# Kernel tuning notes

Hardware: AMD Instinct MI355X
Metric: run time of the kernel (lower is better)

The kernel has to match this reference:

```python
import jax, jax.numpy as jnp
import numpy as np

SHARPNESS = 1000.0   # sigmoid temperature from source: *1000.0
BIAS = 0.008         # shadow acne bias from source: -0.008
FILTER_SIZE = 1      # 3x3 PCF
SHADOW_STEP = 1


def setup_inputs() -> dict:
    key = jax.random.key(0)
    k1, k2, k3 = jax.random.split(key, 3)
    N, H, W, K, S = 8, 1024, 1024, 1, 2048
    # light-view depth buffer (fragments_from_light.zbuf), K=1 squeezed
    light_zbuf = jax.random.uniform(k1, (N, S, S), dtype=jnp.float32)
    depth_z = jax.random.uniform(k2, (N, H, W, K), dtype=jnp.float32)
    # rounded integer light-screen coords per camera pixel: [..., 0]=x, [..., 1]=y
    xy = jax.random.randint(k3, (N, H, W, K, 2), 0, S, dtype=jnp.int32)
    return {"light_zbuf": light_zbuf, "depth_z": depth_z, "xy": xy, "image_size": S}


def reference(light_zbuf, depth_z, xy, image_size):
    N, H, W, K = depth_z.shape
    b = jnp.arange(N, dtype=jnp.int32)[:, None, None, None]  # broadcast batch index
    x = xy[..., 0]  # [N,H,W,K]
    y = xy[..., 1]
    aa = depth_z - BIAS
    vis = jnp.zeros_like(depth_z)
    # 3x3 PCF: gather clamped neighbors in the light zbuf, soft depth test, accumulate
    for ii in range(-FILTER_SIZE, FILTER_SIZE + 1):
        for jj in range(-FILTER_SIZE, FILTER_SIZE + 1):
            yi = jnp.clip(y + ii * SHADOW_STEP, 0, image_size - 1)
            xi = jnp.clip(x + jj * SHADOW_STEP, 0, image_size - 1)
            bb = light_zbuf[b, yi, xi]  # [N,H,W,K] gather
            vis = vis + jax.nn.sigmoid((bb - aa) * SHARPNESS)
    return vis / float((1 + 2 * FILTER_SIZE) ** 2)
```

## Files before the change

### kernel.cpp

```cpp
#include <hip/hip_runtime.h>


#define SHARPNESS 1000.0f
#define BIAS 0.008f
#define S2LOG2E 1442.6950408889634f

#define S_IMG   2048
#define NBATCH  8
#define HWK     (1 << 20)
#define TSH     6
#define TPS     32
#define BPB     (TPS * TPS)
#define CAP     1408
#define RPT     6
#define STW     66
#define PXB     16384
#define P1T     1024
#define PPT     (PXB / P1T)
#define BLKB    (HWK / PXB)
#define SENT    0xFFFFFFFFu

typedef int      i4v __attribute__((ext_vector_type(4)));
typedef float    f2v __attribute__((ext_vector_type(2)));
typedef float    f4v __attribute__((ext_vector_type(4)));
typedef unsigned u2v __attribute__((ext_vector_type(2)));
typedef unsigned u4v __attribute__((ext_vector_type(4)));

__device__ __forceinline__ float sigf(float bb, float a) {
    const float t = (a - bb) * S2LOG2E;
    return __builtin_amdgcn_rcpf(1.0f + exp2f(t));
}

__global__ __launch_bounds__(P1T, 1) void p1_bin(
    const int* __restrict__ xy_raw, const float* __restrict__ depth,
    u2v* __restrict__ slab, float* __restrict__ out ,
    unsigned* __restrict__ gcur, int b0)
{
    __shared__ u2v      srec[PXB];
    __shared__ unsigned scn[BPB];
    __shared__ unsigned lbase[BPB];
    __shared__ unsigned gbse[BPB];

    const int blk = blockIdx.x;
    const int bl  = blk >> 6;
    const int sub = blk & (BLKB - 1);
    const int tid = threadIdx.x;
    scn[tid] = 0;
    __syncthreads();

    const size_t pb_g = (size_t)(b0 + bl) * HWK + (size_t)sub * PXB;
    const i4v* xq = (const i4v*)xy_raw + pb_g / 2;
    const f2v* dq = (const f2v*)depth  + pb_g / 2;

    unsigned pk[PPT]; float dd[PPT];
#pragma unroll
    for (int j = 0; j < PPT / 2; ++j) {
        const i4v q = __builtin_nontemporal_load(&xq[j * P1T + tid]);
        const f2v d = __builtin_nontemporal_load(&dq[j * P1T + tid]);
        pk[2 * j]     = (unsigned)q.x | ((unsigned)q.y << 11);
        pk[2 * j + 1] = (unsigned)q.z | ((unsigned)q.w << 11);
        dd[2 * j] = d.x; dd[2 * j + 1] = d.y;
        atomicAdd(&scn[((q.y >> TSH) << 5) | (q.x >> TSH)], 1u);
        atomicAdd(&scn[((q.w >> TSH) << 5) | (q.z >> TSH)], 1u);
    }
    __syncthreads();

    const unsigned creg = scn[tid];
    for (int ofs = 1; ofs < BPB; ofs <<= 1) {
        const unsigned u = (tid >= ofs) ? scn[tid - ofs] : 0u;
        __syncthreads();
        scn[tid] += u;
        __syncthreads();
    }
    const unsigned lb = scn[tid] - creg;
    lbase[tid] = lb;
    gbse[tid]  = atomicAdd(&gcur[(b0 + bl) * BPB + tid], (creg + 7u) & ~7u);
    scn[tid]   = lb;
    __syncthreads();

    u2v* px2 = (u2v*)(out + pb_g);
#pragma unroll
    for (int j = 0; j < PPT / 2; ++j) {
        u2v pi;
#pragma unroll
        for (int e = 0; e < 2; ++e) {
            const unsigned w = pk[2 * j + e];
            const int x = (int)(w & 0x7FFu), y = (int)(w >> 11);
            const int bn = ((y >> TSH) << 5) | (x >> TSH);
            const unsigned r = atomicAdd(&scn[bn], 1u);
            u2v rec;
            rec.x = (unsigned)(x & 63) | ((unsigned)(y & 63) << 6);
            rec.y = __float_as_uint(dd[2 * j + e]);
            srec[r] = rec;
            const unsigned pos = gbse[bn] + (r - lbase[bn]);
            const unsigned slot = (pos < CAP)
                ? (unsigned)(bl * BPB + bn) * CAP + pos : SENT;
            if (e == 0) pi.x = slot; else pi.y = slot;
        }
        px2[j * P1T + tid] = pi;
    }
    __syncthreads();

    const int wid = tid >> 6, lane = tid & 63;
    u2v* slb = slab + (size_t)bl * BPB * CAP;
    for (int bn = wid * 64; bn < wid * 64 + 64; ++bn) {
        const int c   = (int)(scn[bn] - lbase[bn]);
        const int len = (c + 7) & ~7;
        const int src = (int)lbase[bn];
        const int gp  = (int)gbse[bn];
        u2v* dst = slb + (size_t)bn * CAP;
        for (int k = lane; k < len; k += 64) {
            const int pos = gp + k;
            if (pos < CAP) {
                u2v r;
                if (k < c) r = srec[src + k];
                else { r.x = 0u; r.y = 0x7F800000u; }
                dst[pos] = r;
            }
        }
    }
}

__global__ __launch_bounds__(256, 8) void p2_tile(
    const float* __restrict__ zbuf, u2v* __restrict__ slab,
    const unsigned* __restrict__ gcur, int b0)
{
    __shared__ float zt[STW * STW];
    const int gb  = blockIdx.x;
    const int tid = threadIdx.x;
    const int bl  = gb >> 10;
    const int t   = gb & (BPB - 1);
    const int tx  = t & 31, ty = t >> 5;
    const float* zb = zbuf + (size_t)(b0 + bl) * ((size_t)S_IMG * S_IMG);
    const int x0 = tx * 64 - 1, y0 = ty * 64 - 1;

    const int n   = min((int)gcur[(b0 + bl) * BPB + t], CAP);
    const int nc  = n - 1;
    const int ncc = max(nc, 0);
    u2v* sl = slab + (size_t)gb * CAP;

    u2v Rc[RPT];
#pragma unroll
    for (int j = 0; j < RPT; ++j)
        Rc[j] = sl[min(j * 256 + tid, ncc)];

    for (int i = tid; i < STW * STW; i += 256) {
        const int r  = i / STW, c = i - r * STW;
        const int gy = min(max(y0 + r, 0), S_IMG - 1);
        const int gx = min(max(x0 + c, 0), S_IMG - 1);
        zt[i] = zb[(size_t)gy * S_IMG + gx];
    }
    __syncthreads();

    float* slf = (float*)sl;
#pragma unroll
    for (int j = 0; j < RPT; ++j) {
        const unsigned w = Rc[j].x;
        const float a  = __uint_as_float(Rc[j].y) - BIAS;
        const float* p = zt + (int)((w >> 6) & 63u) * STW + (int)(w & 63u);
        const float v =
              sigf(p[0],           a) + sigf(p[1],           a) + sigf(p[2],           a)
            + sigf(p[STW],         a) + sigf(p[STW + 1],     a) + sigf(p[STW + 2],     a)
            + sigf(p[2 * STW],     a) + sigf(p[2 * STW + 1], a) + sigf(p[2 * STW + 2], a);
        const int k = j * 256 + tid;
        if (k <= nc) slf[2 * k + 1] = v * (1.0f / 9.0f);
    }
}

__global__ __launch_bounds__(256) void p3_out(
    const float* __restrict__ slabf, float* __restrict__ out,
    const float* __restrict__ zbuf, const float* __restrict__ depth,
    const int* __restrict__ xy_raw, int b0)
{
    const int tid = threadIdx.x;
    const size_t pxbase = (size_t)b0 * HWK + (size_t)blockIdx.x * 4096;
    const u4v* px4 = (const u4v*)(out + pxbase);

    u4v P[4];
#pragma unroll
    for (int j = 0; j < 4; ++j)
        P[j] = px4[j * 256 + tid];

    f4v V[4];
#pragma unroll
    for (int j = 0; j < 4; ++j) {
#pragma unroll
        for (int e = 0; e < 4; ++e) {
            const unsigned pi = P[j][e];
            float v;
            if (pi != SENT) {
                v = slabf[2 * (size_t)pi + 1];
            } else {
                const size_t il = pxbase + (size_t)(j * 256 + tid) * 4 + e;
                const int batch = (int)(il >> 20);
                const float a = depth[il] - BIAS;
                const int x = xy_raw[2 * il], y = xy_raw[2 * il + 1];
                const float* zbb = zbuf + (size_t)batch * ((size_t)S_IMG * S_IMG);
                float vv = 0.0f;
                for (int ii = -1; ii <= 1; ++ii) {
                    const int yi = min(max(y + ii, 0), S_IMG - 1);
                    const float* row = zbb + (size_t)yi * S_IMG;
                    for (int jj = -1; jj <= 1; ++jj)
                        vv += sigf(row[min(max(x + jj, 0), S_IMG - 1)], a);
                }
                v = vv * (1.0f / 9.0f);
            }
            V[j][e] = v;
        }
    }

    f4v* o4 = (f4v*)(out + pxbase);
#pragma unroll
    for (int j = 0; j < 4; ++j)
        __builtin_nontemporal_store(V[j], &o4[j * 256 + tid]);
}

__global__ __launch_bounds__(256) void pcf_shadow_generic(
    const float* __restrict__ zbuf, const float* __restrict__ depth_z,
    const int2* __restrict__ xy, const int* __restrict__ image_size_p,
    float* __restrict__ out, int total, int zbuf_elems)
{
    const int i = blockIdx.x * blockDim.x + threadIdx.x;
    if (i >= total) return;
    const int S  = *image_size_p;
    const int SS = S * S;
    const int N  = zbuf_elems / SS;
    const int hwk = total / N;
    const int b   = i / hwk;
    const float a = depth_z[i] - BIAS;
    const int2 p  = xy[i];
    const float* base = zbuf + (size_t)b * (size_t)SS;
    float vis = 0.0f;
#pragma unroll
    for (int ii = -1; ii <= 1; ++ii) {
        const int yi = min(max(p.y + ii, 0), S - 1);
        const float* row = base + (size_t)yi * (size_t)S;
#pragma unroll
        for (int jj = -1; jj <= 1; ++jj) {
            const int xi = min(max(p.x + jj, 0), S - 1);
            vis += 1.0f / (1.0f + __expf((a - row[xi]) * SHARPNESS));
        }
    }
    out[i] = vis * (1.0f / 9.0f);
}

extern "C" void kernel_launch(void* const* d_in, const int* in_sizes, int n_in,
                              void* d_out, int out_size, void* d_ws, size_t ws_size,
                              hipStream_t stream) {
    const float* zbuf     = (const float*)d_in[0];
    const float* depth_z  = (const float*)d_in[1];
    const int*   xy_raw   = (const int*)d_in[2];
    const int*   img_size = (const int*)d_in[3];
    float*       out      = (float*)d_out;

    const int zbuf_elems = in_sizes[0];
    const int total      = in_sizes[1];

    if (zbuf_elems == NBATCH * S_IMG * S_IMG && total == NBATCH * HWK) {
        const size_t slab_pb = (size_t)BPB * CAP * 8ull;
        const size_t gcur_b  = (size_t)NBATCH * BPB * 4ull;
        int nb = 0;
        if      (ws_size >= 8 * slab_pb + gcur_b) nb = 8;
        else if (ws_size >= 4 * slab_pb + gcur_b) nb = 4;
        else if (ws_size >= 2 * slab_pb + gcur_b) nb = 2;
        else if (ws_size >= 1 * slab_pb + gcur_b) nb = 1;

        if (nb) {
            u2v*      slab = (u2v*)d_ws;
            unsigned* gcur = (unsigned*)((char*)d_ws + (size_t)nb * slab_pb);
            hipMemsetAsync(gcur, 0, gcur_b, stream);
            for (int b0 = 0; b0 < NBATCH; b0 += nb) {
                p1_bin <<<nb * BLKB, P1T, 0, stream>>>(xy_raw, depth_z, slab, out, gcur, b0);
                p2_tile<<<nb * BPB,  256, 0, stream>>>(zbuf, slab, gcur, b0);
                p3_out <<<nb * 256,  256, 0, stream>>>((const float*)slab, out,
                                                       zbuf, depth_z, xy_raw, b0);
            }
            return;
        }
    }
    const int block = 256;
    const int grid  = (total + block - 1) / block;
    pcf_shadow_generic<<<grid, block, 0, stream>>>(zbuf, depth_z, (const int2*)xy_raw,
                                                   img_size, out, total, zbuf_elems);
}
```

Measured before the change: 407.0 us.

## Replace per-pixel slot indirection with chunk-binned result pairs scattered in LDS

Pass 1 no longer writes a per-pixel slot index to the output buffer; instead each binned record carries its linear pixel index. Pass 2 computes the 3x3 PCF per tile, then re-bins (pixel, value) pairs by 16K-pixel output chunk into a second workspace. Pass 3 scatters those pairs into shared memory per chunk and writes coalesced output, falling back to a direct gather for overflowed pixels. This removes the random per-pixel gather of slab values in pass 3 and one write/read pass over the output, at the cost of an extra binning step with atomics and a larger workspace. Block sizes and capacities also change (8K pixels per pass-1 block, larger tile capacity).

```diff
diff --git a/kernel.cpp b/kernel.cpp
--- a/kernel.cpp
+++ b/kernel.cpp
@@ -11,30 +11,32 @@
 #define TSH     6
 #define TPS     32
 #define BPB     (TPS * TPS)
-#define CAP     1408
-#define RPT     6
+#define CAP     1664
+#define RPT     7
 #define STW     66
-#define PXB     16384
+#define PXB     8192
 #define P1T     1024
 #define PPT     (PXB / P1T)
-#define BLKB    (HWK / PXB)
+#define P1B     (HWK / PXB)
+#define CHSH    14
+#define NCH     (HWK >> CHSH)
+#define CHPX    (1 << CHSH)
+#define CAP3    21248
 #define SENT    0xFFFFFFFFu
 
 typedef int      i4v __attribute__((ext_vector_type(4)));
 typedef float    f2v __attribute__((ext_vector_type(2)));
 typedef float    f4v __attribute__((ext_vector_type(4)));
 typedef unsigned u2v __attribute__((ext_vector_type(2)));
-typedef unsigned u4v __attribute__((ext_vector_type(4)));
 
 __device__ __forceinline__ float sigf(float bb, float a) {
     const float t = (a - bb) * S2LOG2E;
     return __builtin_amdgcn_rcpf(1.0f + exp2f(t));
 }
 
-__global__ __launch_bounds__(P1T, 1) void p1_bin(
+__global__ __launch_bounds__(P1T, 4) void p1_bin(
     const int* __restrict__ xy_raw, const float* __restrict__ depth,
-    u2v* __restrict__ slab, float* __restrict__ out ,
-    unsigned* __restrict__ gcur, int b0)
+    u2v* __restrict__ slab, unsigned* __restrict__ gcur, int b0)
 {
     __shared__ u2v      srec[PXB];
     __shared__ unsigned scn[BPB];
@@ -42,8 +44,8 @@
     __shared__ unsigned gbse[BPB];
 
     const int blk = blockIdx.x;
-    const int bl  = blk >> 6;
-    const int sub = blk & (BLKB - 1);
+    const int bl  = blk >> 7;
+    const int sub = blk & (P1B - 1);
     const int tid = threadIdx.x;
     scn[tid] = 0;
     __syncthreads();
@@ -78,26 +80,20 @@
     scn[tid]   = lb;
     __syncthreads();
 
-    u2v* px2 = (u2v*)(out + pb_g);
 #pragma unroll
     for (int j = 0; j < PPT / 2; ++j) {
-        u2v pi;
 #pragma unroll
         for (int e = 0; e < 2; ++e) {
             const unsigned w = pk[2 * j + e];
             const int x = (int)(w & 0x7FFu), y = (int)(w >> 11);
             const int bn = ((y >> TSH) << 5) | (x >> TSH);
             const unsigned r = atomicAdd(&scn[bn], 1u);
+            const unsigned il = (unsigned)(sub * PXB + (j * P1T + tid) * 2 + e);
             u2v rec;
-            rec.x = (unsigned)(x & 63) | ((unsigned)(y & 63) << 6);
+            rec.x = il | ((unsigned)(x & 63) << 20) | ((unsigned)(y & 63) << 26);
             rec.y = __float_as_uint(dd[2 * j + e]);
             srec[r] = rec;
-            const unsigned pos = gbse[bn] + (r - lbase[bn]);
-            const unsigned slot = (pos < CAP)
-                ? (unsigned)(bl * BPB + bn) * CAP + pos : SENT;
-            if (e == 0) pi.x = slot; else pi.y = slot;
-        }
-        px2[j * P1T + tid] = pi;
+        }
     }
     __syncthreads();
 
@@ -121,23 +117,29 @@
     }
 }
 
-__global__ __launch_bounds__(256, 8) void p2_tile(
-    const float* __restrict__ zbuf, u2v* __restrict__ slab,
-    const unsigned* __restrict__ gcur, int b0)
+__global__ __launch_bounds__(256, 4) void p2_tile(
+    const float* __restrict__ zbuf, const u2v* __restrict__ slab,
+    u2v* __restrict__ pairs, const unsigned* __restrict__ gcur,
+    unsigned* __restrict__ pcur, int b0)
 {
-    __shared__ float zt[STW * STW];
-    const int gb  = blockIdx.x;
+    __shared__ float    zt[STW * STW];
+    __shared__ u2v      spair[CAP];
+    __shared__ unsigned cnt[NCH], lb[NCH], cur[NCH], gb[NCH];
+
+    const int gbi = blockIdx.x;
     const int tid = threadIdx.x;
-    const int bl  = gb >> 10;
-    const int t   = gb & (BPB - 1);
+    const int bl  = gbi >> 10;
+    const int t   = gbi & (BPB - 1);
     const int tx  = t & 31, ty = t >> 5;
     const float* zb = zbuf + (size_t)(b0 + bl) * ((size_t)S_IMG * S_IMG);
     const int x0 = tx * 64 - 1, y0 = ty * 64 - 1;
 
+    if (tid < NCH) cnt[tid] = 0;
+
     const int n   = min((int)gcur[(b0 + bl) * BPB + t], CAP);
     const int nc  = n - 1;
     const int ncc = max(nc, 0);
-    u2v* sl = slab + (size_t)gb * CAP;
+    const u2v* sl = slab + (size_t)gbi * CAP;
 
     u2v Rc[RPT];
 #pragma unroll
@@ -152,67 +154,112 @@
     }
     __syncthreads();
 
-    float* slf = (float*)sl;
+    float vv[RPT]; unsigned ilv[RPT]; bool val[RPT];
 #pragma unroll
     for (int j = 0; j < RPT; ++j) {
         const unsigned w = Rc[j].x;
+        val[j] = (j * 256 + tid <= nc) && (Rc[j].y != 0x7F800000u);
+        ilv[j] = w & 0xFFFFFu;
         const float a  = __uint_as_float(Rc[j].y) - BIAS;
-        const float* p = zt + (int)((w >> 6) & 63u) * STW + (int)(w & 63u);
-        const float v =
-              sigf(p[0],           a) + sigf(p[1],           a) + sigf(p[2],           a)
-            + sigf(p[STW],         a) + sigf(p[STW + 1],     a) + sigf(p[STW + 2],     a)
-            + sigf(p[2 * STW],     a) + sigf(p[2 * STW + 1], a) + sigf(p[2 * STW + 2], a);
-        const int k = j * 256 + tid;
-        if (k <= nc) slf[2 * k + 1] = v * (1.0f / 9.0f);
-    }
-}
-
-__global__ __launch_bounds__(256) void p3_out(
-    const float* __restrict__ slabf, float* __restrict__ out,
+        const float* p = zt + (int)((w >> 26) & 63u) * STW + (int)((w >> 20) & 63u);
+        vv[j] = (sigf(p[0],           a) + sigf(p[1],           a) + sigf(p[2],           a)
+               + sigf(p[STW],         a) + sigf(p[STW + 1],     a) + sigf(p[STW + 2],     a)
+               + sigf(p[2 * STW],     a) + sigf(p[2 * STW + 1], a) + sigf(p[2 * STW + 2], a))
+              * (1.0f / 9.0f);
+        if (val[j]) atomicAdd(&cnt[ilv[j] >> CHSH], 1u);
+    }
+    __syncthreads();
+
+    if (tid == 0) {
+        unsigned s = 0;
+        for (int c = 0; c < NCH; ++c) { lb[c] = s; s += cnt[c]; }
+    }
+    __syncthreads();
+    if (tid < NCH) {
+        cur[tid] = lb[tid];
+        gb[tid]  = atomicAdd(&pcur[(b0 + bl) * NCH + tid], (cnt[tid] + 7u) & ~7u);
+    }
+    __syncthreads();
+
+#pragma unroll
+    for (int j = 0; j < RPT; ++j) {
+        if (val[j]) {
+            const unsigned c = ilv[j] >> CHSH;
+            const unsigned r = atomicAdd(&cur[c], 1u);
+            u2v pr; pr.x = ilv[j]; pr.y = __float_as_uint(vv[j]);
+            spair[r] = pr;
+        }
+    }
+    __syncthreads();
+
+    const int wid = tid >> 6, lane = tid & 63;
+    u2v* pb = pairs + (size_t)bl * NCH * CAP3;
+    for (int c = wid * 16; c < wid * 16 + 16; ++c) {
+        const int cc  = (int)cnt[c];
+        const int len = (cc + 7) & ~7;
+        const int src = (int)lb[c];
+        const int gp  = (int)gb[c];
+        u2v* dst = pb + (size_t)c * CAP3;
+        for (int k = lane; k < len; k += 64) {
+            const int pos = gp + k;
+            if (pos < CAP3) {
+                u2v pr;
+                if (k < cc) pr = spair[src + k];
+                else { pr.x = SENT; pr.y = 0u; }
+                dst[pos] = pr;
+            }
+        }
+    }
+}
+
+__global__ __launch_bounds__(1024, 4) void p3_out(
+    const u2v* __restrict__ pairs, const unsigned* __restrict__ pcur,
+    float* __restrict__ out,
     const float* __restrict__ zbuf, const float* __restrict__ depth,
     const int* __restrict__ xy_raw, int b0)
 {
+    __shared__ float sd[CHPX];
+    const int blk = blockIdx.x;
+    const int bl  = blk >> 6;
+    const int c   = blk & (NCH - 1);
     const int tid = threadIdx.x;
-    const size_t pxbase = (size_t)b0 * HWK + (size_t)blockIdx.x * 4096;
-    const u4v* px4 = (const u4v*)(out + pxbase);
-
-    u4v P[4];
-#pragma unroll
-    for (int j = 0; j < 4; ++j)
-        P[j] = px4[j * 256 + tid];
-
-    f4v V[4];
+
+    for (int i = tid; i < CHPX; i += 1024) sd[i] = -1.0f;
+    __syncthreads();
+
+    const int nlist = min((int)pcur[(b0 + bl) * NCH + c], CAP3);
+    const u2v* pl = pairs + ((size_t)bl * NCH + c) * CAP3;
+    for (int k = tid; k < nlist; k += 1024) {
+        const u2v pr = pl[k];
+        if (pr.x != SENT) sd[pr.x & (CHPX - 1)] = __uint_as_float(pr.y);
+    }
+    __syncthreads();
+
+    const size_t pxb = (size_t)(b0 + bl) * HWK + (size_t)c * CHPX;
 #pragma unroll
     for (int j = 0; j < 4; ++j) {
+        const int idx = (j * 1024 + tid) * 4;
+        f4v v = *(const f4v*)(sd + idx);
 #pragma unroll
         for (int e = 0; e < 4; ++e) {
-            const unsigned pi = P[j][e];
-            float v;
-            if (pi != SENT) {
-                v = slabf[2 * (size_t)pi + 1];
-            } else {
-                const size_t il = pxbase + (size_t)(j * 256 + tid) * 4 + e;
+            if (v[e] < 0.0f) {
+                const size_t il = pxb + (size_t)idx + e;
                 const int batch = (int)(il >> 20);
                 const float a = depth[il] - BIAS;
                 const int x = xy_raw[2 * il], y = xy_raw[2 * il + 1];
                 const float* zbb = zbuf + (size_t)batch * ((size_t)S_IMG * S_IMG);
-                float vv = 0.0f;
+                float vr = 0.0f;
                 for (int ii = -1; ii <= 1; ++ii) {
                     const int yi = min(max(y + ii, 0), S_IMG - 1);
                     const float* row = zbb + (size_t)yi * S_IMG;
                     for (int jj = -1; jj <= 1; ++jj)
-                        vv += sigf(row[min(max(x + jj, 0), S_IMG - 1)], a);
+                        vr += sigf(row[min(max(x + jj, 0), S_IMG - 1)], a);
                 }
-                v = vv * (1.0f / 9.0f);
+                v[e] = vr * (1.0f / 9.0f);
             }
-            V[j][e] = v;
-        }
-    }
-
-    f4v* o4 = (f4v*)(out + pxbase);
-#pragma unroll
-    for (int j = 0; j < 4; ++j)
-        __builtin_nontemporal_store(V[j], &o4[j * 256 + tid]);
+        }
+        __builtin_nontemporal_store(v, (f4v*)(out + pxb) + j * 1024 + tid);
+    }
 }
 
 __global__ __launch_bounds__(256) void pcf_shadow_generic(
@@ -257,22 +304,27 @@
     const int total      = in_sizes[1];
 
     if (zbuf_elems == NBATCH * S_IMG * S_IMG && total == NBATCH * HWK) {
-        const size_t slab_pb = (size_t)BPB * CAP * 8ull;
-        const size_t gcur_b  = (size_t)NBATCH * BPB * 4ull;
+        const size_t slab_pb  = (size_t)BPB * CAP * 8ull;
+        const size_t pairs_pb = (size_t)NCH * CAP3 * 8ull;
+        const size_t per_b    = slab_pb + pairs_pb;
+        const size_t ctr_b    = (size_t)NBATCH * BPB * 4ull
+                              + (size_t)NBATCH * NCH * 4ull;
         int nb = 0;
-        if      (ws_size >= 8 * slab_pb + gcur_b) nb = 8;
-        else if (ws_size >= 4 * slab_pb + gcur_b) nb = 4;
-        else if (ws_size >= 2 * slab_pb + gcur_b) nb = 2;
-        else if (ws_size >= 1 * slab_pb + gcur_b) nb = 1;
+        if      (ws_size >= 8 * per_b + ctr_b) nb = 8;
+        else if (ws_size >= 4 * per_b + ctr_b) nb = 4;
+        else if (ws_size >= 2 * per_b + ctr_b) nb = 2;
+        else if (ws_size >= 1 * per_b + ctr_b) nb = 1;
 
         if (nb) {
-            u2v*      slab = (u2v*)d_ws;
-            unsigned* gcur = (unsigned*)((char*)d_ws + (size_t)nb * slab_pb);
-            hipMemsetAsync(gcur, 0, gcur_b, stream);
+            u2v*      slab  = (u2v*)d_ws;
+            u2v*      pairs = (u2v*)((char*)d_ws + (size_t)nb * slab_pb);
+            unsigned* gcur  = (unsigned*)((char*)d_ws + (size_t)nb * per_b);
+            unsigned* pcur  = gcur + (size_t)NBATCH * BPB;
+            hipMemsetAsync(gcur, 0, ctr_b, stream);
             for (int b0 = 0; b0 < NBATCH; b0 += nb) {
-                p1_bin <<<nb * BLKB, P1T, 0, stream>>>(xy_raw, depth_z, slab, out, gcur, b0);
-                p2_tile<<<nb * BPB,  256, 0, stream>>>(zbuf, slab, gcur, b0);
-                p3_out <<<nb * 256,  256, 0, stream>>>((const float*)slab, out,
+                p1_bin <<<nb * P1B, P1T,  0, stream>>>(xy_raw, depth_z, slab, gcur, b0);
+                p2_tile<<<nb * BPB, 256,  0, stream>>>(zbuf, slab, pairs, gcur, pcur, b0);
+                p3_out <<<nb * NCH, 1024, 0, stream>>>(pairs, pcur, out,
                                                        zbuf, depth_z, xy_raw, b0);
             }
             return;
```

Measured after the change: 440.2 us. +8.2%, slower.
